# Kernel tuning notes

Measured on AMD Instinct MI355X. Metric: run time of the kernel, lower is better.

The kernel has to match this reference:

```python
import jax, jax.numpy as jnp
import numpy as np

B, S, D = 2, 2048, 1280
H = 20
HD = D // H  # 64, rotary dim


def setup_inputs() -> dict:
    key = jax.random.key(0)
    ks = jax.random.split(key, 4)
    scale = 0.02
    return {
        "hidden_states": jax.random.normal(ks[0], (B, S, D), jnp.float32),
        "Wq": jax.random.normal(ks[1], (D, D), jnp.float32) * scale,
        "bq": jnp.zeros((D,), jnp.float32),
        "Wk": jax.random.normal(ks[2], (D, D), jnp.float32) * scale,
        "bk": jnp.zeros((D,), jnp.float32),
        "Wv": jax.random.normal(ks[3], (D, D), jnp.float32) * scale,
        "bv": jnp.zeros((D,), jnp.float32),
    }


def _rotate_half(x):
    x1, x2 = jnp.split(x, 2, axis=-1)
    return jnp.concatenate((-x2, x1), axis=-1)


def _rotary_cos_sin(seq_len, dim, dtype):
    inv_freq = 1.0 / (10000.0 ** (jnp.arange(0, dim, 2, dtype=jnp.float32) / dim))
    t = jnp.arange(seq_len, dtype=jnp.float32)
    freqs = jnp.einsum("i,j->ij", t, inv_freq)          # [S, dim/2]
    emb = jnp.concatenate((freqs, freqs), axis=-1)        # [S, dim]
    return jnp.cos(emb).astype(dtype)[None, None], jnp.sin(emb).astype(dtype)[None, None]


def reference(hidden_states, Wq, bq, Wk, bk, Wv, bv):
    b, s, d = hidden_states.shape
    # QKV projections, split heads -> [B, H, S, HD]
    def proj(W, bias):
        y = hidden_states @ W + bias
        return y.reshape(b, s, H, HD).transpose(0, 2, 1, 3)

    q = proj(Wq, bq) * (HD ** -0.5)  # scale BEFORE rotary, as in source
    k = proj(Wk, bk)
    v = proj(Wv, bv)

    cos, sin = _rotary_cos_sin(s, HD, q.dtype)
    q = q * cos + _rotate_half(q) * sin
    k = k * cos + _rotate_half(k) * sin

    scores = jnp.einsum("bhqd,bhkd->bhqk", q, k)
    probs = jax.nn.softmax(scores, axis=-1)
    ctx = jnp.einsum("bhqk,bhkd->bhqd", probs, v)
    return ctx.transpose(0, 2, 1, 3).reshape(b, s, d)
```

## Files before the change

### kernel.cpp

```cpp
#include <hip/hip_runtime.h>

#define DD 1280
#define SS 2048
#define HH 20

typedef __bf16 bf16x8 __attribute__((ext_vector_type(8)));
typedef float f32x4 __attribute__((ext_vector_type(4)));

typedef __attribute__((address_space(3))) unsigned int lds_uint;
typedef __attribute__((address_space(1))) unsigned int glb_uint;
#define GLL16(g, l) __builtin_amdgcn_global_load_lds((const glb_uint*)(g), (lds_uint*)(l), 16, 0, 0)

__device__ __forceinline__ unsigned short f2bf(float f) {
  union { float f; unsigned u; } v; v.f = f;
  unsigned r = v.u + 0x7fffu + ((v.u >> 16) & 1u);
  return (unsigned short)(r >> 16);
}
__device__ __forceinline__ unsigned f2u(float f) {
  union { float f; unsigned u; } v; v.f = f; return v.u;
}
__device__ __forceinline__ float u2f(unsigned x) {
  union { unsigned u; float f; } v; v.u = x; return v.f;
}
__device__ __forceinline__ unsigned pk2(float lo, float hi) {
  return ((unsigned)f2bf(hi) << 16) | (unsigned)f2bf(lo);
}

__global__ __launch_bounds__(256) void prep_kernel(
    const float* __restrict__ X, const float* __restrict__ Wq,
    const float* __restrict__ Wk, const float* __restrict__ Wv,
    unsigned short* __restrict__ Xb, unsigned short* __restrict__ WT,
    float2* __restrict__ cs) {
  __shared__ __align__(8) unsigned short tile[64][68];
  int bid = blockIdx.x, tid = threadIdx.x;
  if (bid < 320) {
#pragma unroll
    for (int it = 0; it < 8; it++) {
      size_t base = (size_t)(it * 320 + bid) * 2048 + (size_t)tid * 8;
      const float4* xin = (const float4*)(X + base);
      float4 a = xin[0], c = xin[1];
      uint4 o = make_uint4(pk2(a.x, a.y), pk2(a.z, a.w), pk2(c.x, c.y), pk2(c.z, c.w));
      *(uint4*)(Xb + base) = o;
    }
  } else if (bid < 1520) {
    int wb = bid - 320;
    int mat = wb / 400;
    int t = wb % 400;
    int tn = t % 20, tk = t / 20;
    const float* W = (mat == 0) ? Wq : ((mat == 1) ? Wk : Wv);
    int k0 = tk * 64, n0 = tn * 64;
    int r = tid >> 2, cq = tid & 3;
    const float* src = W + (size_t)(k0 + r) * DD + n0 + cq * 16;
#pragma unroll
    for (int j = 0; j < 4; j++) {
      float4 wv = *(const float4*)(src + j * 4);
      *(ushort4*)&tile[r][cq * 16 + j * 4] =
          make_ushort4(f2bf(wv.x), f2bf(wv.y), f2bf(wv.z), f2bf(wv.w));
    }
    __syncthreads();
    unsigned short* out = WT + (size_t)mat * DD * DD + (size_t)(n0 + r) * DD + k0 + cq * 16;
#pragma unroll
    for (int j = 0; j < 4; j++) {
      ushort4 o = make_ushort4(tile[cq * 16 + j * 4 + 0][r], tile[cq * 16 + j * 4 + 1][r],
                               tile[cq * 16 + j * 4 + 2][r], tile[cq * 16 + j * 4 + 3][r]);
      *(ushort4*)(out + j * 4) = o;
    }
  } else {
#pragma unroll
    for (int it = 0; it < 4; it++) {
      int idx = (bid - 1520) * 1024 + it * 256 + tid;
      int sp = idx >> 5, j = idx & 31;
      float invf = exp2f(-(float)j * 0.41524101186092034f);
      float ang = (float)sp * invf;
      cs[idx] = make_float2(cosf(ang), sinf(ang));
    }
  }
}

__global__ __launch_bounds__(256) void qkv_gemm_kernel(
    const unsigned short* __restrict__ Xb, const unsigned short* __restrict__ WT,
    const float* __restrict__ bq, const float* __restrict__ bk, const float* __restrict__ bv,
    const float2* __restrict__ cs,
    unsigned short* __restrict__ Qr, unsigned short* __restrict__ Kr,
    unsigned short* __restrict__ VT) {
  __shared__ __align__(16) unsigned short As[128 * 32];
  __shared__ __align__(16) unsigned short Bs[128 * 32];
  int bx0 = blockIdx.x;
  int bx = (bx0 & 7) * 120 + (bx0 >> 3);
  int mat = bx / 320;
  int r0 = bx % 320;
  int tm = r0 / 10, tn = r0 % 10;
  int m0 = tm * 128, n0 = tn * 128;
  int tid = threadIdx.x;
  int lane = tid & 63, wave = tid >> 6;
  int c15 = lane & 15, quad = lane >> 4;
  int wm = wave >> 1, wn = wave & 1;
  const unsigned short* Wm = WT + (size_t)mat * DD * DD;

  int rowA = tid >> 2;
  int c8 = (tid & 3) * 8;
  const unsigned short* gA0 = Xb + (size_t)(m0 + rowA) * DD + c8;
  const unsigned short* gA1 = gA0 + (size_t)64 * DD;
  const unsigned short* gB0 = Wm + (size_t)(n0 + rowA) * DD + c8;
  const unsigned short* gB1 = gB0 + (size_t)64 * DD;
  unsigned short* ldsA0 = As + wave * 512;
  unsigned short* ldsA1 = As + 2048 + wave * 512;
  unsigned short* ldsB0 = Bs + wave * 512;
  unsigned short* ldsB1 = Bs + 2048 + wave * 512;

  f32x4 acc[4][4] = {};

  for (int kk = 0; kk < DD; kk += 32) {
    __syncthreads();
    GLL16(gA0 + kk, ldsA0);
    GLL16(gA1 + kk, ldsA1);
    GLL16(gB0 + kk, ldsB0);
    GLL16(gB1 + kk, ldsB1);
    __syncthreads();
    bf16x8 af[4];
#pragma unroll
    for (int mi = 0; mi < 4; mi++)
      af[mi] = *(const bf16x8*)(As + (wm * 64 + mi * 16 + c15) * 32 + quad * 8);
#pragma unroll
    for (int ni = 0; ni < 4; ni++) {
      bf16x8 bfr = *(const bf16x8*)(Bs + (wn * 64 + ni * 16 + c15) * 32 + quad * 8);
#pragma unroll
      for (int mi = 0; mi < 4; mi++)
        acc[mi][ni] = __builtin_amdgcn_mfma_f32_16x16x32_bf16(af[mi], bfr, acc[mi][ni], 0, 0, 0);
    }
  }

  int growb = m0 + wm * 64;
  int gcolb = n0 + wn * 64;
  if (mat == 2) {
#pragma unroll
    for (int mi = 0; mi < 4; mi++) {
      int row0 = growb + mi * 16 + quad * 4;
      int bb_ = row0 >> 11, sp = row0 & 2047;
#pragma unroll
      for (int ni = 0; ni < 4; ni++) {
        int gcol = gcolb + ni * 16 + c15;
        float bias = bv[gcol];
        int hh = gcol >> 6, dd = gcol & 63;
        f32x4 v = acc[mi][ni];
        ushort4 o = make_ushort4(f2bf(v[0] + bias), f2bf(v[1] + bias),
                                 f2bf(v[2] + bias), f2bf(v[3] + bias));
        *(ushort4*)(VT + ((size_t)((bb_ * HH + hh) * 64 + dd)) * SS + sp) = o;
      }
    }
  } else {
    unsigned short* Out = (mat == 0) ? Qr : Kr;
    const float* bias = (mat == 0) ? bq : bk;
    float qs = (mat == 0) ? 0.18033688011112042f : 1.0f;
#pragma unroll
    for (int mi = 0; mi < 4; mi++) {
      int row0 = growb + mi * 16 + quad * 4;
#pragma unroll
      for (int ni = 0; ni < 2; ni++) {
        int gcol_lo = gcolb + ni * 16 + c15;
        int gcol_hi = gcol_lo + 32;
        float blo = bias[gcol_lo], bhi = bias[gcol_hi];
        int d = ni * 16 + c15;
        f32x4 lo = acc[mi][ni], hi = acc[mi][ni + 2];
#pragma unroll
        for (int r = 0; r < 4; r++) {
          int grow = row0 + r;
          float2 cv = cs[(size_t)(grow & 2047) * 32 + d];
          float xl = (lo[r] + blo) * qs, xh = (hi[r] + bhi) * qs;
          Out[(size_t)grow * DD + gcol_lo] = f2bf(xl * cv.x - xh * cv.y);
          Out[(size_t)grow * DD + gcol_hi] = f2bf(xh * cv.x + xl * cv.y);
        }
      }
    }
  }
}

__global__ __launch_bounds__(256)
void attn_kernel(
    const unsigned short* __restrict__ Qr, const unsigned short* __restrict__ Kr,
    const unsigned short* __restrict__ VT, float* __restrict__ out) {
  __shared__ __align__(16) unsigned short Klds[3][2048];
  __shared__ __align__(16) unsigned short Vlds[3][2048];
  int bx = blockIdx.x;
  int bh = bx % 40, qt = bx / 40;
  int b = bh / HH, h = bh % HH;
  int tid = threadIdx.x;
  int lane = tid & 63, w = tid >> 6;
  int c15 = lane & 15, quad = lane >> 4;
  int q0 = qt * 64 + w * 16;

  const unsigned short* Qb = Qr + (size_t)(b * SS + q0 + c15) * DD + h * 64 + quad * 8;
  bf16x8 qf[2];
  qf[0] = *(const bf16x8*)(Qb);
  qf[1] = *(const bf16x8*)(Qb + 32);

  int krow = tid >> 3, kch = tid & 7;
  const unsigned short* Ksrc = Kr + (size_t)(b * SS + krow) * DD + h * 64
                               + ((kch ^ (krow & 7)) * 8);
  int vrow = tid >> 2, vch = tid & 3;
  const unsigned short* Vsrc = VT + (size_t)(bh * 64 + vrow) * SS
                               + ((vch ^ ((vrow >> 1) & 3)) * 8);

  f32x4 of[4] = {};
  float ol = 0.f;

  GLL16(Ksrc,                    &Klds[0][0] + w * 512);
  GLL16(Vsrc,                    &Vlds[0][0] + w * 512);
  GLL16(Ksrc + (size_t)32 * DD,  &Klds[1][0] + w * 512);
  GLL16(Vsrc + 32,               &Vlds[1][0] + w * 512);
  asm volatile("s_waitcnt vmcnt(2)" ::: "memory");
  __builtin_amdgcn_sched_barrier(0);
  __builtin_amdgcn_s_barrier();

  for (int t = 0; t < 64; t++) {
    int cur = t % 3;
    if (t + 2 < 64) {
      int nxt = (t + 2) % 3;
      GLL16(Ksrc + (size_t)((t + 2) * 32) * DD, &Klds[nxt][0] + w * 512);
      GLL16(Vsrc + (t + 2) * 32,                &Vlds[nxt][0] + w * 512);
    }
    const unsigned short* Kb = &Klds[cur][0];
    const unsigned short* Vb = &Vlds[cur][0];

    f32x4 sc[2] = {};
#pragma unroll
    for (int kc = 0; kc < 2; kc++)
#pragma unroll
      for (int ni = 0; ni < 2; ni++) {
        int R = ni * 16 + c15;
        bf16x8 kf = *(const bf16x8*)(Kb + R * 64 + (((kc * 4 + quad) ^ (R & 7)) * 8));
        sc[ni] = __builtin_amdgcn_mfma_f32_16x16x32_bf16(kf, qf[kc], sc[ni], 0, 0, 0);
      }

    unsigned e0 = f2u(__builtin_amdgcn_exp2f(sc[0][0]));
    unsigned e1 = f2u(__builtin_amdgcn_exp2f(sc[0][1]));
    unsigned e2 = f2u(__builtin_amdgcn_exp2f(sc[0][2]));
    unsigned e3 = f2u(__builtin_amdgcn_exp2f(sc[0][3]));
    unsigned e4 = f2u(__builtin_amdgcn_exp2f(sc[1][0]));
    unsigned e5 = f2u(__builtin_amdgcn_exp2f(sc[1][1]));
    unsigned e6 = f2u(__builtin_amdgcn_exp2f(sc[1][2]));
    unsigned e7 = f2u(__builtin_amdgcn_exp2f(sc[1][3]));
    union { unsigned u[4]; bf16x8 v; } af;
    af.u[0] = (e1 & 0xffff0000u) | (e0 >> 16);
    af.u[1] = (e3 & 0xffff0000u) | (e2 >> 16);
    af.u[2] = (e5 & 0xffff0000u) | (e4 >> 16);
    af.u[3] = (e7 & 0xffff0000u) | (e6 >> 16);
    {
      float s01 = u2f(e0 & 0xffff0000u) + u2f(e1 & 0xffff0000u);
      float s23 = u2f(e2 & 0xffff0000u) + u2f(e3 & 0xffff0000u);
      float s45 = u2f(e4 & 0xffff0000u) + u2f(e5 & 0xffff0000u);
      float s67 = u2f(e6 & 0xffff0000u) + u2f(e7 & 0xffff0000u);
      ol += (s01 + s23) + (s45 + s67);
    }

#pragma unroll
    for (int nio = 0; nio < 4; nio++) {
      int R = nio * 16 + c15;
      int f = (R >> 1) & 3;
      union { ushort4 s[2]; bf16x8 v; } vf;
      vf.s[0] = *(const ushort4*)(Vb + R * 32 + ((((quad >> 1)) ^ f) * 8) + (quad & 1) * 4);
      vf.s[1] = *(const ushort4*)(Vb + R * 32 + (((2 + (quad >> 1)) ^ f) * 8) + (quad & 1) * 4);
      of[nio] = __builtin_amdgcn_mfma_f32_16x16x32_bf16(af.v, vf.v, of[nio], 0, 0, 0);
    }

    if (t + 2 < 64) {
      asm volatile("s_waitcnt vmcnt(2)" ::: "memory");
    } else {
      asm volatile("s_waitcnt vmcnt(0)" ::: "memory");
    }
    __builtin_amdgcn_sched_barrier(0);
    __builtin_amdgcn_s_barrier();
  }

  float lt = ol;
  lt += __shfl_xor(lt, 16);
  lt += __shfl_xor(lt, 32);

#pragma unroll
  for (int r = 0; r < 4; r++) {
    float lq = __shfl(lt, quad * 4 + r);
    float invl = 1.0f / lq;
    float* op = out + (size_t)(b * SS + q0 + quad * 4 + r) * DD + h * 64 + c15;
#pragma unroll
    for (int nio = 0; nio < 4; nio++)
      op[nio * 16] = of[nio][r] * invl;
  }
}

extern "C" void kernel_launch(void* const* d_in, const int* in_sizes, int n_in,
                              void* d_out, int out_size, void* d_ws, size_t ws_size,
                              hipStream_t stream) {
  (void)in_sizes; (void)n_in; (void)out_size; (void)ws_size;
  const float* X  = (const float*)d_in[0];
  const float* Wq = (const float*)d_in[1];
  const float* bq = (const float*)d_in[2];
  const float* Wk = (const float*)d_in[3];
  const float* bk = (const float*)d_in[4];
  const float* Wv = (const float*)d_in[5];
  const float* bv = (const float*)d_in[6];
  char* ws = (char*)d_ws;
  unsigned short* Xb  = (unsigned short*)(ws);
  unsigned short* WT  = (unsigned short*)(ws + 10485760);
  unsigned short* Qr  = (unsigned short*)(ws + 20316160);
  unsigned short* Kr  = (unsigned short*)(ws + 30801920);
  unsigned short* VTt = (unsigned short*)(ws + 41287680);
  float2* cstab       = (float2*)(ws + 51773440);
  hipLaunchKernelGGL(prep_kernel, dim3(1584), dim3(256), 0, stream, X, Wq, Wk, Wv, Xb, WT, cstab);
  hipLaunchKernelGGL(qkv_gemm_kernel, dim3(960), dim3(256), 0, stream, Xb, WT, bq, bk, bv, cstab, Qr, Kr, VTt);
  hipLaunchKernelGGL(attn_kernel, dim3(1280), dim3(256), 0, stream, Qr, Kr, VTt, (float*)d_out);
}
```

Before: 227.4 us.

## Triple-buffer QKV GEMM LDS tiles with async prefetch and XOR swizzle

Turns the QKV projection GEMM main loop into a three-stage pipeline. Global-to-LDS loads run two K-steps ahead, and there is one barrier per iteration gated by explicit vmcnt waits instead of two full syncs. It also XOR-swizzles the column chunk per row, both in the global source offsets and in the LDS reads, to cut LDS bank conflicts. LDS use triples, which may lower occupancy, and correctness now depends on the hand-placed waitcnt counts.

```diff
diff --git a/kernel.cpp b/kernel.cpp
--- a/kernel.cpp
+++ b/kernel.cpp
@@ -83,8 +83,8 @@
     const float2* __restrict__ cs,
     unsigned short* __restrict__ Qr, unsigned short* __restrict__ Kr,
     unsigned short* __restrict__ VT) {
-  __shared__ __align__(16) unsigned short As[128 * 32];
-  __shared__ __align__(16) unsigned short Bs[128 * 32];
+  __shared__ __align__(16) unsigned short As[3][4096];
+  __shared__ __align__(16) unsigned short Bs[3][4096];
   int bx0 = blockIdx.x;
   int bx = (bx0 & 7) * 120 + (bx0 >> 3);
   int mat = bx / 320;
@@ -98,37 +98,55 @@
   const unsigned short* Wm = WT + (size_t)mat * DD * DD;
 
   int rowA = tid >> 2;
-  int c8 = (tid & 3) * 8;
-  const unsigned short* gA0 = Xb + (size_t)(m0 + rowA) * DD + c8;
+  int sc8 = ((tid & 3) ^ ((tid >> 3) & 3)) * 8;
+  const unsigned short* gA0 = Xb + (size_t)(m0 + rowA) * DD + sc8;
   const unsigned short* gA1 = gA0 + (size_t)64 * DD;
-  const unsigned short* gB0 = Wm + (size_t)(n0 + rowA) * DD + c8;
+  const unsigned short* gB0 = Wm + (size_t)(n0 + rowA) * DD + sc8;
   const unsigned short* gB1 = gB0 + (size_t)64 * DD;
-  unsigned short* ldsA0 = As + wave * 512;
-  unsigned short* ldsA1 = As + 2048 + wave * 512;
-  unsigned short* ldsB0 = Bs + wave * 512;
-  unsigned short* ldsB1 = Bs + 2048 + wave * 512;
 
   f32x4 acc[4][4] = {};
 
-  for (int kk = 0; kk < DD; kk += 32) {
-    __syncthreads();
-    GLL16(gA0 + kk, ldsA0);
-    GLL16(gA1 + kk, ldsA1);
-    GLL16(gB0 + kk, ldsB0);
-    GLL16(gB1 + kk, ldsB1);
-    __syncthreads();
+#define STAGE(P, KK)                                          \
+  {                                                           \
+    GLL16(gA0 + (KK), &As[P][0] + wave * 512);                \
+    GLL16(gA1 + (KK), &As[P][0] + 2048 + wave * 512);         \
+    GLL16(gB0 + (KK), &Bs[P][0] + wave * 512);                \
+    GLL16(gB1 + (KK), &Bs[P][0] + 2048 + wave * 512);         \
+  }
+
+  STAGE(0, 0)
+  STAGE(1, 32)
+  asm volatile("s_waitcnt vmcnt(4)" ::: "memory");
+  __builtin_amdgcn_sched_barrier(0);
+  __builtin_amdgcn_s_barrier();
+
+  for (int t = 0; t < 40; t++) {
+    if (t + 2 < 40) STAGE((t + 2) % 3, (t + 2) * 32)
+    const unsigned short* Ab = &As[t % 3][0];
+    const unsigned short* Bb = &Bs[t % 3][0];
     bf16x8 af[4];
 #pragma unroll
-    for (int mi = 0; mi < 4; mi++)
-      af[mi] = *(const bf16x8*)(As + (wm * 64 + mi * 16 + c15) * 32 + quad * 8);
+    for (int mi = 0; mi < 4; mi++) {
+      int row = wm * 64 + mi * 16 + c15;
+      af[mi] = *(const bf16x8*)(Ab + row * 32 + ((quad ^ ((row >> 1) & 3)) * 8));
+    }
 #pragma unroll
     for (int ni = 0; ni < 4; ni++) {
-      bf16x8 bfr = *(const bf16x8*)(Bs + (wn * 64 + ni * 16 + c15) * 32 + quad * 8);
+      int rowb = wn * 64 + ni * 16 + c15;
+      bf16x8 bfr = *(const bf16x8*)(Bb + rowb * 32 + ((quad ^ ((rowb >> 1) & 3)) * 8));
 #pragma unroll
       for (int mi = 0; mi < 4; mi++)
         acc[mi][ni] = __builtin_amdgcn_mfma_f32_16x16x32_bf16(af[mi], bfr, acc[mi][ni], 0, 0, 0);
     }
-  }
+    if (t + 2 < 40) {
+      asm volatile("s_waitcnt vmcnt(4)" ::: "memory");
+    } else {
+      asm volatile("s_waitcnt vmcnt(0)" ::: "memory");
+    }
+    __builtin_amdgcn_sched_barrier(0);
+    __builtin_amdgcn_s_barrier();
+  }
+#undef STAGE
 
   int growb = m0 + wm * 64;
   int gcolb = n0 + wn * 64;
```

After: 227.5 us. No clear change (+0.0%).
